# Kernel tuning notes

Measured on AMD Instinct MI355X. Metric: run time of the kernel, lower is better.

## Reference

```python
import jax, jax.numpy as jnp
import numpy as np

B, NQ, NK = 4, 2048, 2048
DQ = DK = DV = 512
H = 8
DS = DV // H  # 64


def _layernorm(x, g, b, eps=1e-5):
    m = jnp.mean(x, axis=-1, keepdims=True)
    v = jnp.var(x, axis=-1, keepdims=True)
    return (x - m) * jax.lax.rsqrt(v + eps) * g + b


def setup_inputs() -> dict:
    key = jax.random.key(0)
    ks = jax.random.split(key, 16)
    def lin(k, fan_in, fan_out):
        # torch nn.Linear default init: U(-1/sqrt(fan_in), 1/sqrt(fan_in))
        bound = 1.0 / np.sqrt(fan_in)
        k1, k2 = jax.random.split(k)
        W = jax.random.uniform(k1, (fan_in, fan_out), jnp.float32, -bound, bound)
        b = jax.random.uniform(k2, (fan_out,), jnp.float32, -bound, bound)
        return W, b
    Wq, bq = lin(ks[0], DQ, DV)
    Wk, bk = lin(ks[1], DK, DV)
    Wv, bv = lin(ks[2], DK, DV)
    W0, b0 = lin(ks[3], DV, DV)
    W1, b1 = lin(ks[4], DV, DV)
    # xavier_uniform for kp/vp of shape (1, DS): bound = sqrt(6/(1+DS))
    xb = np.sqrt(6.0 / (1 + DS))
    kp = jax.random.uniform(ks[5], (DS,), jnp.float32, -xb, xb)
    vp = jax.random.uniform(ks[6], (DS,), jnp.float32, -xb, xb)
    return {
        "Q": jax.random.normal(ks[7], (B, NQ, DQ), jnp.float32),
        "K": jax.random.normal(ks[8], (B, NK, DK), jnp.float32),
        "Kpos": jax.random.uniform(ks[9], (B, NQ, NK), jnp.float32),
        "Wq": Wq, "bq": bq, "Wk": Wk, "bk": bk, "Wv": Wv, "bv": bv,
        "kp": kp, "vp": vp,
        "W0": W0, "b0": b0, "W1": W1, "b1": b1,
        "g0": jnp.ones((DV,), jnp.float32), "be0": jnp.zeros((DV,), jnp.float32),
        "g1": jnp.ones((DV,), jnp.float32), "be1": jnp.zeros((DV,), jnp.float32),
    }


def reference(Q, K, Kpos, Wq, bq, Wk, bk, Wv, bv, kp, vp, W0, b0, W1, b1, g0, be0, g1, be1):
    Qp = Q @ Wq + bq                       # [B,NQ,DV]
    Kp = K @ Wk + bk                       # [B,NK,DV]
    Vp = K @ Wv + bv                       # [B,NK,DV]
    # head split (torch split/cat along batch == reshape to [B,N,H,DS])
    Qh = Qp.reshape(B, NQ, H, DS)
    Kh = Kp.reshape(B, NK, H, DS)
    Vh = Vp.reshape(B, NK, H, DS)
    scale = 1.0 / np.sqrt(DV)              # NOTE: original scales by sqrt(dim_V), not per-head dim
    scores = jnp.einsum('bqhd,bkhd->bhqk', Qh, Kh) * scale
    # ShawRE key bias: KE[b,h,q,k] = Kpos[b,q,k] * <Qh[b,q,h,:], kp>
    qkp = jnp.einsum('bqhd,d->bhq', Qh, kp)          # [B,H,NQ]
    scores = scores + Kpos[:, None, :, :] * qkp[:, :, :, None]
    A = jax.nn.softmax(scores, axis=-1)              # [B,H,NQ,NK]
    out = jnp.einsum('bhqk,bkhd->bqhd', A, Vh)       # [B,NQ,H,DS]
    # ShawRE value bias: VE[b,q,h,:] = (sum_k A*Kpos) * vp
    akp = jnp.einsum('bhqk,bqk->bhq', A, Kpos)       # [B,H,NQ]
    out = out + akp.transpose(0, 2, 1)[..., None] * vp
    O = (Qh + out).reshape(B, NQ, DV)
    O = _layernorm(O, g0, be0)
    resO = O
    O = jax.nn.relu(O @ W0 + b0)           # fc_o[0] with relu (numlayers=2)
    O = resO + jax.nn.relu(O @ W1 + b1)    # fc_o[-1] + residual
    O = _layernorm(O, g1, be1)
    return O
```

## Files before the change

### kernel.cpp

```cpp
#include <hip/hip_runtime.h>
#include <math.h>

#define Bx  4
#define NQx 2048
#define NKx 2048
#define Dx  512
#define Hx  8

typedef __attribute__((ext_vector_type(8))) __bf16 bf16x8;
typedef __attribute__((ext_vector_type(4))) float f32x4;
typedef __attribute__((ext_vector_type(16))) float f32x16;

typedef const __attribute__((address_space(1))) unsigned int* gas_ptr;
typedef __attribute__((address_space(3))) unsigned int* lds_ptr;

__device__ __forceinline__ void gload16(const void* g, void* l){
  __builtin_amdgcn_global_load_lds((gas_ptr)g, (lds_ptr)l, 16, 0, 0);
}

__device__ __forceinline__ unsigned short f2bf(float f){
  union { float f; unsigned int u; } v; v.f = f;
  unsigned int r = (v.u + 0x7FFFu + ((v.u >> 16) & 1u)) >> 16;
  return (unsigned short)r;
}
__device__ __forceinline__ float bf2f(unsigned short u){
  union { unsigned int u; float f; } v; v.u = ((unsigned int)u) << 16; return v.f;
}
__device__ __forceinline__ unsigned int cvtpk_bf16(float a, float b){
  unsigned int d;
  asm("v_cvt_pk_bf16_f32 %0, %1, %2" : "=v"(d) : "v"(a), "v"(b));
  return d;
}
__device__ __forceinline__ void plane32_swap(unsigned int& a, unsigned int& b){
  asm("v_permlane32_swap_b32 %0, %1" : "+v"(a), "+v"(b));
}
__device__ __forceinline__ float fexp2(float x){
  float d; asm("v_exp_f32 %0, %1" : "=v"(d) : "v"(x)); return d;
}
__device__ __forceinline__ float fmax3(float a, float b, float c){
  float d; asm("v_max3_f32 %0, %1, %2, %3" : "=v"(d) : "v"(a), "v"(b), "v"(c)); return d;
}

__global__ __launch_bounds__(256) void mab_wt(
    const float* __restrict__ Wq, const float* __restrict__ Wk, const float* __restrict__ Wv,
    const float* __restrict__ W0, const float* __restrict__ W1,
    unsigned short* __restrict__ Wt)
{
  __shared__ unsigned short T[64][72];
  const int z = blockIdx.z;
  const float* W = (z==0)?Wq:(z==1)?Wk:(z==2)?Wv:(z==3)?W0:W1;
  unsigned short* O = Wt + (size_t)z*512*512;
  const int k0 = blockIdx.x*64, n0 = blockIdx.y*64;
  const int tid = threadIdx.x;
  #pragma unroll
  for (int i=0;i<4;++i){
    int id = tid + i*256;
    int r = id>>4, c4 = id&15;
    float4 v = *(const float4*)(W + (size_t)(k0+r)*512 + n0 + c4*4);
    ushort4 o; o.x=f2bf(v.x); o.y=f2bf(v.y); o.z=f2bf(v.z); o.w=f2bf(v.w);
    *(ushort4*)&T[r][c4*4] = o;
  }
  __syncthreads();
  #pragma unroll
  for (int i=0;i<2;++i){
    int id = tid + i*256;
    int c = id>>3, r8 = id&7;
    union { unsigned short u[8]; uint4 v; } o;
    #pragma unroll
    for (int j=0;j<8;++j) o.u[j] = T[r8*8+j][c];
    *(uint4*)(O + (size_t)(n0+c)*512 + k0 + r8*8) = o.v;
  }
}

__global__ __launch_bounds__(256) void mab_vt(
    const unsigned short* __restrict__ Vp, unsigned short* __restrict__ Vpt)
{
  __shared__ unsigned short T[64][72];
  const int r0 = blockIdx.x*64;
  const int c0 = blockIdx.y*64;
  const int b  = blockIdx.z;
  const int tid = threadIdx.x;
  #pragma unroll
  for (int i=0;i<2;++i){
    int id = tid + i*256;
    int r = id>>3, c8 = id&7;
    *(uint4*)&T[r][c8*8] = *(const uint4*)(Vp + (size_t)(b*NKx + r0+r)*512 + c0 + c8*8);
  }
  __syncthreads();
  #pragma unroll
  for (int i=0;i<2;++i){
    int id = tid + i*256;
    int c = id>>3, r8 = id&7;
    union { unsigned short u[8]; uint4 v; } o;
    #pragma unroll
    for (int j=0;j<8;++j) o.u[j] = T[r8*8+j][c];
    *(uint4*)(Vpt + ((size_t)(b*512) + c0 + c)*NKx + r0 + r8*8) = o.v;
  }
}

__global__ __launch_bounds__(256) void mab_gemm_proj(
    const float* __restrict__ Qf, const float* __restrict__ Kf,
    const unsigned short* __restrict__ Wt,
    const float* __restrict__ bq, const float* __restrict__ bk, const float* __restrict__ bv,
    unsigned short* __restrict__ Cb, float kscale)
{
  __shared__ unsigned short As[128][64];
  __shared__ unsigned short Bs[128][64];
  const int z = blockIdx.z;
  const float* A = (z==0) ? Qf : Kf;
  const unsigned short* W = Wt + (size_t)z*512*512;
  const float* bias = (z==0)?bq:((z==1)?bk:bv);
  const float sc = (z==1) ? kscale : 1.0f;
  const int m0 = blockIdx.y*128, n0 = blockIdx.x*128;
  const int tid = threadIdx.x, w = tid>>6, lane = tid&63, g = lane>>4, q16 = lane&15;
  const int wr = w>>1, wc = w&1;

  f32x4 acc[4][4];
  #pragma unroll
  for (int m=0;m<4;++m)
    #pragma unroll
    for (int n=0;n<4;++n) acc[m][n] = (f32x4){0.f,0.f,0.f,0.f};

  float4 areg[8];
  #pragma unroll
  for (int i=0;i<8;++i){
    int id = i*256 + tid, row = id>>4, qc = id&15;
    areg[i] = *(const float4*)(A + (size_t)(m0+row)*512 + qc*4);
  }

  for (int k0 = 0; k0 < 512; k0 += 64){
    __syncthreads();
    #pragma unroll
    for (int i=0;i<8;++i){
      int id = i*256 + tid, row = id>>4, qc = id&15;
      unsigned int lo = cvtpk_bf16(areg[i].x, areg[i].y);
      unsigned int hi = cvtpk_bf16(areg[i].z, areg[i].w);
      unsigned int* dst = (unsigned int*)((char*)&As[0][0] + row*128
                          + ((qc>>1) ^ (row&7))*16 + (qc&1)*8);
      dst[0] = lo; dst[1] = hi;
    }
    #pragma unroll
    for (int i=0;i<4;++i){
      int o   = (w*4 + i)*1024 + lane*16;
      int row = o >> 7;
      int c   = (o >> 4) & 7;
      int cs  = c ^ (row & 7);
      gload16(W + (size_t)(n0+row)*512 + k0 + cs*8, (char*)&Bs[0][0] + (w*4+i)*1024);
    }
    __syncthreads();
    if (k0 + 64 < 512){
      #pragma unroll
      for (int i=0;i<8;++i){
        int id = i*256 + tid, row = id>>4, qc = id&15;
        areg[i] = *(const float4*)(A + (size_t)(m0+row)*512 + (k0+64) + qc*4);
      }
    }
    #pragma unroll
    for (int ks=0;ks<2;++ks){
      bf16x8 af[4], bfr[4];
      #pragma unroll
      for (int m=0;m<4;++m){
        int row = wr*64 + m*16 + q16;
        int c   = (ks*4 + g) ^ (row & 7);
        af[m] = *(const bf16x8*)((const char*)&As[0][0] + row*128 + c*16);
      }
      #pragma unroll
      for (int n=0;n<4;++n){
        int row = wc*64 + n*16 + q16;
        int c   = (ks*4 + g) ^ (row & 7);
        bfr[n] = *(const bf16x8*)((const char*)&Bs[0][0] + row*128 + c*16);
      }
      #pragma unroll
      for (int m=0;m<4;++m)
        #pragma unroll
        for (int n=0;n<4;++n)
          acc[m][n] = __builtin_amdgcn_mfma_f32_16x16x32_bf16(af[m], bfr[n], acc[m][n], 0,0,0);
    }
  }

  const size_t ZS = (size_t)8192*512;
  #pragma unroll
  for (int m=0;m<4;++m){
    const int rowl = wr*64 + m*16 + g*4;
    #pragma unroll
    for (int n=0;n<4;++n){
      const int col = n0 + wc*64 + n*16 + q16;
      const float bv2 = bias[col];
      #pragma unroll
      for (int r=0;r<4;++r){
        float v = (acc[m][n][r] + bv2) * sc;
        Cb[(size_t)z*ZS + (size_t)(m0 + rowl + r)*512 + col] = f2bf(v);
      }
    }
  }
}

__global__ __launch_bounds__(256) void mab_gemm_mfma(
    const unsigned short* __restrict__ A, const unsigned short* __restrict__ W,
    const float* __restrict__ bias, const float* __restrict__ res,
    unsigned short* __restrict__ Cb, float* __restrict__ Cf, int relu)
{
  __shared__ unsigned short As[128][64];
  __shared__ unsigned short Bs[128][64];
  const int m0 = blockIdx.y*128, n0 = blockIdx.x*128;
  const int tid = threadIdx.x, w = tid>>6, lane = tid&63, g = lane>>4, q16 = lane&15;
  const int wr = w>>1, wc = w&1;

  f32x4 acc[4][4];
  #pragma unroll
  for (int m=0;m<4;++m)
    #pragma unroll
    for (int n=0;n<4;++n) acc[m][n] = (f32x4){0.f,0.f,0.f,0.f};

  for (int k0 = 0; k0 < 512; k0 += 64){
    __syncthreads();
    #pragma unroll
    for (int i=0;i<4;++i){
      int o   = (w*4 + i)*1024 + lane*16;
      int row = o >> 7;
      int c   = (o >> 4) & 7;
      int cs  = c ^ (row & 7);
      gload16(A + (size_t)(m0+row)*512 + k0 + cs*8, (char*)&As[0][0] + (w*4+i)*1024);
      gload16(W + (size_t)(n0+row)*512 + k0 + cs*8, (char*)&Bs[0][0] + (w*4+i)*1024);
    }
    __syncthreads();
    #pragma unroll
    for (int ks=0;ks<2;++ks){
      bf16x8 af[4], bfr[4];
      #pragma unroll
      for (int m=0;m<4;++m){
        int row = wr*64 + m*16 + q16;
        int c   = (ks*4 + g) ^ (row & 7);
        af[m] = *(const bf16x8*)((const char*)&As[0][0] + row*128 + c*16);
      }
      #pragma unroll
      for (int n=0;n<4;++n){
        int row = wc*64 + n*16 + q16;
        int c   = (ks*4 + g) ^ (row & 7);
        bfr[n] = *(const bf16x8*)((const char*)&Bs[0][0] + row*128 + c*16);
      }
      #pragma unroll
      for (int m=0;m<4;++m)
        #pragma unroll
        for (int n=0;n<4;++n)
          acc[m][n] = __builtin_amdgcn_mfma_f32_16x16x32_bf16(af[m], bfr[n], acc[m][n], 0,0,0);
    }
  }

  #pragma unroll
  for (int m=0;m<4;++m){
    const int rowl = wr*64 + m*16 + g*4;
    #pragma unroll
    for (int n=0;n<4;++n){
      const int col = n0 + wc*64 + n*16 + q16;
      const float bv = bias[col];
      #pragma unroll
      for (int r=0;r<4;++r){
        float v = acc[m][n][r] + bv;
        if (relu) v = fmaxf(v, 0.f);
        size_t off = (size_t)(m0 + rowl + r)*512 + col;
        if (res) v += res[off];
        if (Cb) Cb[off] = f2bf(v);
        if (Cf) Cf[off] = v;
      }
    }
  }
}

__global__ __launch_bounds__(256, 4) void mab_attn3(
    const unsigned short* __restrict__ Qp, const unsigned short* __restrict__ Kp,
    const unsigned short* __restrict__ Vpt,
    const float* __restrict__ Kpos, const float* __restrict__ kp, const float* __restrict__ vp,
    float* __restrict__ X)
{
  __shared__ __align__(16) char pool[32768];

  const int q0 = blockIdx.x*64;
  const int h  = blockIdx.y;
  const int b  = blockIdx.z;
  const int tid = threadIdx.x, w = tid>>6, lane = tid&63;
  const int q32 = lane & 31, hi = lane >> 5;
  const int g = w>>1;
  const int qrow = (w&1)*32 + q32;

  char* Kbase = pool + g*16384;
  char* Vbase = pool + g*16384 + 8192;

  const unsigned short* Qg = Qp + ((size_t)(b*NQx + q0))*Dx + h*64;
  const unsigned short* Kg = Kp + ((size_t)b*NKx)*Dx + h*64;
  const unsigned short* Vg = Vpt + ((size_t)(b*512) + h*64)*NKx;
  const float* KProw = Kpos + (size_t)b*NQx*NKx + (size_t)(q0 + qrow)*NKx;

  const int krow0 = lane>>3, kch = lane&7;
  const int vrow0 = lane>>2, vch = lane&3;
  const int shalf = (w&1)*2;

  #pragma unroll
  for (int i=0;i<2;++i){
    int s = shalf + i;
    int kr = s*8 + krow0;
    int kcs = kch ^ (kr & 7);
    gload16(Kg + (size_t)(g*32 + kr)*Dx + kcs*8, Kbase + s*1024);
    int vr = s*16 + vrow0;
    int vcs = vch ^ ((vr>>1) & 3);
    gload16(Vg + (size_t)vr*NKx + g*32 + vcs*8, Vbase + s*1024);
  }

  const unsigned short* Qrowp = Qg + (size_t)qrow*Dx;
  bf16x8 qf[4];
  #pragma unroll
  for (int ds=0; ds<4; ++ds)
    qf[ds] = *(const bf16x8*)(Qrowp + ds*16 + hi*8);

  float qkp = 0.f;
  #pragma unroll
  for (int ds=0; ds<4; ++ds){
    union { bf16x8 v; unsigned short u[8]; } qa; qa.v = qf[ds];
    #pragma unroll
    for (int j=0;j<8;++j)
      qkp = fmaf(bf2f(qa.u[j]), kp[ds*16 + hi*8 + j], qkp);
  }
  qkp += __shfl_xor(qkp, 32);
  qkp *= 1.4426950408889634f;

  float m_i = -1e30f, l_i = 0.f, a_i = 0.f;
  f32x16 accT[2];
  #pragma unroll
  for (int db=0; db<2; ++db)
    #pragma unroll
    for (int r=0;r<16;++r) accT[db][r] = 0.f;

  __syncthreads();

  for (int t = 0; t < 32; ++t){
    const int cur = t & 1;
    const int k0g = t*64 + g*32;

    f32x4 kq[4];
    #pragma unroll
    for (int a=0;a<4;++a)
      kq[a] = *(const f32x4*)(KProw + k0g + a*8 + hi*4);

    if (t < 31){
      const int k1 = k0g + 64;
      #pragma unroll
      for (int i=0;i<2;++i){
        int s = shalf + i;
        int kr = s*8 + krow0;
        int kcs = kch ^ (kr & 7);
        gload16(Kg + (size_t)(k1 + kr)*Dx + kcs*8, Kbase + (cur^1)*4096 + s*1024);
        int vr = s*16 + vrow0;
        int vcs = vch ^ ((vr>>1) & 3);
        gload16(Vg + (size_t)vr*NKx + k1 + vcs*8, Vbase + (cur^1)*4096 + s*1024);
      }
    }
    __builtin_amdgcn_sched_barrier(0);

    f32x16 sT;
    #pragma unroll
    for (int r=0;r<16;++r) sT[r] = 0.f;
    __builtin_amdgcn_s_setprio(1);
    #pragma unroll
    for (int ds=0; ds<4; ++ds){
      int cc = (ds*2 + hi) ^ (q32 & 7);
      bf16x8 kf = *(const bf16x8*)(Kbase + cur*4096 + q32*128 + cc*16);
      sT = __builtin_amdgcn_mfma_f32_32x32x16_bf16(kf, qf[ds], sT, 0,0,0);
    }
    __builtin_amdgcn_s_setprio(0);

    #pragma unroll
    for (int r=0;r<16;++r)
      sT[r] = fmaf(kq[r>>2][r&3], qkp, sT[r]);

    float p0 = fmax3(sT[0],  sT[1],  sT[2]);
    float p1 = fmax3(sT[3],  sT[4],  sT[5]);
    float p2 = fmax3(sT[6],  sT[7],  sT[8]);
    float p3 = fmax3(sT[9],  sT[10], sT[11]);
    float p4 = fmax3(sT[12], sT[13], sT[14]);
    float rm = fmax3(fmax3(p0, p1, p2), fmax3(p3, p4, sT[15]), m_i);
    rm = fmaxf(rm, __shfl_xor(rm, 32));

    if (!__all(rm <= m_i + 11.544f)){
      float al = fexp2(m_i - rm);
      m_i = rm;
      l_i *= al; a_i *= al;
      #pragma unroll
      for (int db=0; db<2; ++db)
        #pragma unroll
        for (int r=0;r<16;++r) accT[db][r] *= al;
    }

    float ps = 0.f, pk = 0.f;
    #pragma unroll
    for (int r=0;r<16;++r){
      float p = fexp2(sT[r] - m_i);
      sT[r] = p;
      ps += p;
      pk = fmaf(p, kq[r>>2][r&3], pk);
    }
    ps += __shfl_xor(ps, 32);
    pk += __shfl_xor(pk, 32);
    l_i += ps; a_i += pk;

    union PW { unsigned int u[4]; bf16x8 v; } pa[2];
    {
      unsigned int w0 = cvtpk_bf16(sT[0],  sT[1]);
      unsigned int w1 = cvtpk_bf16(sT[2],  sT[3]);
      unsigned int w2 = cvtpk_bf16(sT[4],  sT[5]);
      unsigned int w3 = cvtpk_bf16(sT[6],  sT[7]);
      unsigned int w4 = cvtpk_bf16(sT[8],  sT[9]);
      unsigned int w5 = cvtpk_bf16(sT[10], sT[11]);
      unsigned int w6 = cvtpk_bf16(sT[12], sT[13]);
      unsigned int w7 = cvtpk_bf16(sT[14], sT[15]);
      plane32_swap(w0, w2);
      plane32_swap(w1, w3);
      plane32_swap(w4, w6);
      plane32_swap(w5, w7);
      pa[0].u[0]=w0; pa[0].u[1]=w1; pa[0].u[2]=w2; pa[0].u[3]=w3;
      pa[1].u[0]=w4; pa[1].u[1]=w5; pa[1].u[2]=w6; pa[1].u[3]=w7;
    }

    __builtin_amdgcn_s_setprio(1);
    #pragma unroll
    for (int c2=0; c2<2; ++c2){
      #pragma unroll
      for (int db=0; db<2; ++db){
        int row = db*32 + q32;
        int cc  = (c2*2 + hi) ^ ((row>>1) & 3);
        bf16x8 vf = *(const bf16x8*)(Vbase + cur*4096 + row*64 + cc*16);
        accT[db] = __builtin_amdgcn_mfma_f32_32x32x16_bf16(vf, pa[c2].v, accT[db], 0,0,0);
      }
    }
    __builtin_amdgcn_s_setprio(0);

    __syncthreads();
  }

  __syncthreads();
  float* mp = (float*)pool;
  {
    int slot = w*64 + lane;
    float* ms = mp + slot*20;
    int send = 1 - g;
    #pragma unroll
    for (int r=0;r<16;++r) ms[r] = accT[send][r];
    ms[16] = m_i; ms[17] = l_i; ms[18] = a_i;
  }
  __syncthreads();
  {
    int pslot = (w^2)*64 + lane;
    const float* pp = mp + pslot*20;
    float pm = pp[16], pl = pp[17], pav = pp[18];
    float mM = fmaxf(m_i, pm);
    float alS = fexp2(m_i - mM), alP = fexp2(pm - mM);
    float lM = fmaf(l_i, alS, pl*alP);
    float aM = fmaf(a_i, alS, pav*alP);
    float inv = 1.0f / lM;
    float aw  = aM * inv;
    float* Xrow = X + ((size_t)(b*NQx + q0 + qrow))*Dx + h*64;
    #pragma unroll
    for (int a2=0; a2<4; ++a2){
      int d0 = g*32 + a2*8 + hi*4;
      f32x4 vpv = *(const f32x4*)(vp + d0);
      ushort4 qh = *(const ushort4*)(Qrowp + d0);
      float4 o;
      o.x = fmaf(fmaf(accT[g][a2*4+0], alS, pp[a2*4+0]*alP), inv, bf2f(qh.x) + aw*vpv[0]);
      o.y = fmaf(fmaf(accT[g][a2*4+1], alS, pp[a2*4+1]*alP), inv, bf2f(qh.y) + aw*vpv[1]);
      o.z = fmaf(fmaf(accT[g][a2*4+2], alS, pp[a2*4+2]*alP), inv, bf2f(qh.z) + aw*vpv[2]);
      o.w = fmaf(fmaf(accT[g][a2*4+3], alS, pp[a2*4+3]*alP), inv, bf2f(qh.w) + aw*vpv[3]);
      *(float4*)(Xrow + d0) = o;
    }
  }
}

__global__ __launch_bounds__(256) void mab_ln2(
    const float* __restrict__ Xin, const float* __restrict__ g,
    const float* __restrict__ be, float* __restrict__ Yf, unsigned short* __restrict__ Yb)
{
  const int row = blockIdx.x;
  const int tid = threadIdx.x;
  const float* x = Xin + (size_t)row*Dx;
  float2 v = *(const float2*)(x + tid*2);
  float s  = v.x + v.y;
  float sq = fmaf(v.x,v.x, v.y*v.y);
  #pragma unroll
  for (int m=1; m<64; m<<=1){ s += __shfl_xor(s,m); sq += __shfl_xor(sq,m); }
  __shared__ float red[2][4];
  const int wid = tid>>6, lane = tid&63;
  if (lane==0){ red[0][wid]=s; red[1][wid]=sq; }
  __syncthreads();
  s  = red[0][0]+red[0][1]+red[0][2]+red[0][3];
  sq = red[1][0]+red[1][1]+red[1][2]+red[1][3];
  float mean = s*(1.0f/Dx);
  float var  = sq*(1.0f/Dx) - mean*mean;
  float rstd = rsqrtf(var + 1e-5f);
  float2 gg = *(const float2*)(g  + tid*2);
  float2 bb = *(const float2*)(be + tid*2);
  float2 o;
  o.x = (v.x-mean)*rstd*gg.x + bb.x;
  o.y = (v.y-mean)*rstd*gg.y + bb.y;
  if (Yf) *(float2*)(Yf + (size_t)row*Dx + tid*2) = o;
  if (Yb){
    ushort2 ob; ob.x = f2bf(o.x); ob.y = f2bf(o.y);
    *(ushort2*)(Yb + (size_t)row*Dx + tid*2) = ob;
  }
}

extern "C" void kernel_launch(void* const* d_in, const int* in_sizes, int n_in,
                              void* d_out, int out_size, void* d_ws, size_t ws_size,
                              hipStream_t stream)
{
  const float* Q    = (const float*)d_in[0];
  const float* K    = (const float*)d_in[1];
  const float* Kpos = (const float*)d_in[2];
  const float* Wq   = (const float*)d_in[3];
  const float* bq   = (const float*)d_in[4];
  const float* Wk   = (const float*)d_in[5];
  const float* bk   = (const float*)d_in[6];
  const float* Wv   = (const float*)d_in[7];
  const float* bv   = (const float*)d_in[8];
  const float* kp   = (const float*)d_in[9];
  const float* vp   = (const float*)d_in[10];
  const float* W0   = (const float*)d_in[11];
  const float* b0   = (const float*)d_in[12];
  const float* W1   = (const float*)d_in[13];
  const float* b1   = (const float*)d_in[14];
  const float* g0   = (const float*)d_in[15];
  const float* be0  = (const float*)d_in[16];
  const float* g1   = (const float*)d_in[17];
  const float* be1  = (const float*)d_in[18];
  float* out = (float*)d_out;
  char* wsb  = (char*)d_ws;

  const size_t MB = 1024*1024;
  unsigned short* Qp  = (unsigned short*)(wsb);
  unsigned short* Kp  = (unsigned short*)(wsb + 8*MB);
  unsigned short* Vp  = (unsigned short*)(wsb + 16*MB);
  float*          O0  = (float*)         (wsb + 24*MB);
  unsigned short* Vpt = (unsigned short*)(wsb + 40*MB);
  unsigned short* O0b = (unsigned short*)(wsb + 48*MB);
  unsigned short* Wt  = (unsigned short*)(wsb + 56*MB);
  unsigned short* T1  = Vp;

  const float kscale = 0.044194173824159216f * 1.4426950408889634f;

  mab_wt<<<dim3(8,8,5), 256, 0, stream>>>(Wq, Wk, Wv, W0, W1, Wt);
  mab_gemm_proj<<<dim3(4,64,3), 256, 0, stream>>>(Q, K, Wt, bq, bk, bv, Qp, kscale);
  mab_vt<<<dim3(32,8,4), 256, 0, stream>>>(Vp, Vpt);
  mab_attn3<<<dim3(32,8,4), 256, 0, stream>>>(Qp, Kp, Vpt, Kpos, kp, vp, out);
  mab_ln2<<<8192, 256, 0, stream>>>(out, g0, be0, O0, O0b);
  mab_gemm_mfma<<<dim3(4,64,1), 256, 0, stream>>>(
      O0b, Wt + (size_t)3*512*512, b0, nullptr, T1, nullptr, 1);
  mab_gemm_mfma<<<dim3(4,64,1), 256, 0, stream>>>(
      T1, Wt + (size_t)4*512*512, b1, O0, nullptr, out, 1);
  mab_ln2<<<8192, 256, 0, stream>>>(out, g1, be1, out, nullptr);
}
```

Before: 217.8 us.

## Share Kpos tile across all heads in one block; use bf16 residual

The attention kernel is reorganised so each 512-thread block handles 32 queries for all 8 heads, one wave per head. The Kpos tile is staged once in LDS and read by every head, rather than each head block re-reading Kpos from global memory. This removes the 8x redundant Kpos traffic and the cross-wave split-K merge, at the cost of about 136KB of LDS per block and only 256 blocks. The post-LN fp32 copy is dropped, so the residual add now reads the bf16 LN output, which lowers precision on the residual path.

```diff
diff --git a/kernel.cpp b/kernel.cpp
--- a/kernel.cpp
+++ b/kernel.cpp
@@ -197,7 +197,7 @@
 
 __global__ __launch_bounds__(256) void mab_gemm_mfma(
     const unsigned short* __restrict__ A, const unsigned short* __restrict__ W,
-    const float* __restrict__ bias, const float* __restrict__ res,
+    const float* __restrict__ bias, const unsigned short* __restrict__ resb,
     unsigned short* __restrict__ Cb, float* __restrict__ Cf, int relu)
 {
   __shared__ unsigned short As[128][64];
@@ -259,7 +259,7 @@
         float v = acc[m][n][r] + bv;
         if (relu) v = fmaxf(v, 0.f);
         size_t off = (size_t)(m0 + rowl + r)*512 + col;
-        if (res) v += res[off];
+        if (resb) v += bf2f(resb[off]);
         if (Cb) Cb[off] = f2bf(v);
         if (Cf) Cf[off] = v;
       }
@@ -267,46 +267,45 @@
   }
 }
 
-__global__ __launch_bounds__(256, 4) void mab_attn3(
+__global__ __launch_bounds__(512, 2) void mab_attn7(
     const unsigned short* __restrict__ Qp, const unsigned short* __restrict__ Kp,
     const unsigned short* __restrict__ Vpt,
     const float* __restrict__ Kpos, const float* __restrict__ kp, const float* __restrict__ vp,
     float* __restrict__ X)
 {
-  __shared__ __align__(16) char pool[32768];
-
-  const int q0 = blockIdx.x*64;
-  const int h  = blockIdx.y;
-  const int b  = blockIdx.z;
+  __shared__ __align__(16) char pool[139264];
+
+  const int qt = blockIdx.x;
+  const int b  = blockIdx.y;
+  const int q0 = qt*32;
   const int tid = threadIdx.x, w = tid>>6, lane = tid&63;
   const int q32 = lane & 31, hi = lane >> 5;
-  const int g = w>>1;
-  const int qrow = (w&1)*32 + q32;
-
-  char* Kbase = pool + g*16384;
-  char* Vbase = pool + g*16384 + 8192;
-
-  const unsigned short* Qg = Qp + ((size_t)(b*NQx + q0))*Dx + h*64;
+  const int h = w;
+
+  char* Kbase = pool + w*8192;
+  char* Vbase = pool + 65536 + w*8192;
+  char* KQb   = pool + 131072;
+
   const unsigned short* Kg = Kp + ((size_t)b*NKx)*Dx + h*64;
   const unsigned short* Vg = Vpt + ((size_t)(b*512) + h*64)*NKx;
-  const float* KProw = Kpos + (size_t)b*NQx*NKx + (size_t)(q0 + qrow)*NKx;
-
-  const int krow0 = lane>>3, kch = lane&7;
-  const int vrow0 = lane>>2, vch = lane&3;
-  const int shalf = (w&1)*2;
-
-  #pragma unroll
-  for (int i=0;i<2;++i){
-    int s = shalf + i;
-    int kr = s*8 + krow0;
-    int kcs = kch ^ (kr & 7);
-    gload16(Kg + (size_t)(g*32 + kr)*Dx + kcs*8, Kbase + s*1024);
-    int vr = s*16 + vrow0;
-    int vcs = vch ^ ((vr>>1) & 3);
-    gload16(Vg + (size_t)vr*NKx + g*32 + vcs*8, Vbase + s*1024);
-  }
-
-  const unsigned short* Qrowp = Qg + (size_t)qrow*Dx;
+  const float* KPg = Kpos + (size_t)b*NQx*NKx + (size_t)q0*NKx;
+
+  const int sr8 = lane>>3, sc8 = lane&7;
+  const int sr4 = lane>>2, sc4 = lane&3;
+
+  #pragma unroll
+  for (int i=0;i<4;++i){
+    int kr = i*8 + sr8, kcs = sc8 ^ (kr & 7);
+    gload16(Kg + (size_t)kr*Dx + kcs*8, Kbase + i*1024);
+    int vr = i*16 + sr4, vcs = sc4 ^ ((vr>>1) & 3);
+    gload16(Vg + (size_t)vr*NKx + vcs*8, Vbase + i*1024);
+  }
+  if (w < 4){
+    int pr = w*8 + sr8, pcs = sc8 ^ (pr & 7);
+    gload16(KPg + (size_t)pr*NKx + pcs*4, KQb + w*1024);
+  }
+
+  const unsigned short* Qrowp = Qp + ((size_t)(b*NQx + q0 + q32))*Dx + h*64;
   bf16x8 qf[4];
   #pragma unroll
   for (int ds=0; ds<4; ++ds)
@@ -332,26 +331,22 @@
 
   __syncthreads();
 
-  for (int t = 0; t < 32; ++t){
+  for (int t = 0; t < 64; ++t){
     const int cur = t & 1;
-    const int k0g = t*64 + g*32;
-
-    f32x4 kq[4];
-    #pragma unroll
-    for (int a=0;a<4;++a)
-      kq[a] = *(const f32x4*)(KProw + k0g + a*8 + hi*4);
-
-    if (t < 31){
-      const int k1 = k0g + 64;
-      #pragma unroll
-      for (int i=0;i<2;++i){
-        int s = shalf + i;
-        int kr = s*8 + krow0;
-        int kcs = kch ^ (kr & 7);
-        gload16(Kg + (size_t)(k1 + kr)*Dx + kcs*8, Kbase + (cur^1)*4096 + s*1024);
-        int vr = s*16 + vrow0;
-        int vcs = vch ^ ((vr>>1) & 3);
-        gload16(Vg + (size_t)vr*NKx + k1 + vcs*8, Vbase + (cur^1)*4096 + s*1024);
+    const int k0 = t*32;
+
+    if (t+1 < 64){
+      const int k1 = k0 + 32;
+      #pragma unroll
+      for (int i=0;i<4;++i){
+        int kr = i*8 + sr8, kcs = sc8 ^ (kr & 7);
+        gload16(Kg + (size_t)(k1 + kr)*Dx + kcs*8, Kbase + (cur^1)*4096 + i*1024);
+        int vr = i*16 + sr4, vcs = sc4 ^ ((vr>>1) & 3);
+        gload16(Vg + (size_t)vr*NKx + k1 + vcs*8, Vbase + (cur^1)*4096 + i*1024);
+      }
+      if (w < 4){
+        int pr = w*8 + sr8, pcs = sc8 ^ (pr & 7);
+        gload16(KPg + (size_t)pr*NKx + k1 + pcs*4, KQb + (cur^1)*4096 + w*1024);
       }
     }
     __builtin_amdgcn_sched_barrier(0);
@@ -368,16 +363,23 @@
     }
     __builtin_amdgcn_s_setprio(0);
 
+    f32x4 kq[4];
+    #pragma unroll
+    for (int a=0;a<4;++a){
+      int cc = (a*2 + hi) ^ (q32 & 7);
+      kq[a] = *(const f32x4*)(KQb + cur*4096 + q32*128 + cc*16);
+    }
+
     #pragma unroll
     for (int r=0;r<16;++r)
       sT[r] = fmaf(kq[r>>2][r&3], qkp, sT[r]);
 
-    float p0 = fmax3(sT[0],  sT[1],  sT[2]);
-    float p1 = fmax3(sT[3],  sT[4],  sT[5]);
-    float p2 = fmax3(sT[6],  sT[7],  sT[8]);
-    float p3 = fmax3(sT[9],  sT[10], sT[11]);
-    float p4 = fmax3(sT[12], sT[13], sT[14]);
-    float rm = fmax3(fmax3(p0, p1, p2), fmax3(p3, p4, sT[15]), m_i);
+    float t0 = fmax3(sT[0],  sT[1],  sT[2]);
+    float t1 = fmax3(sT[3],  sT[4],  sT[5]);
+    float t2 = fmax3(sT[6],  sT[7],  sT[8]);
+    float t3 = fmax3(sT[9],  sT[10], sT[11]);
+    float t4 = fmax3(sT[12], sT[13], sT[14]);
+    float rm = fmax3(fmax3(t0, t1, t2), fmax3(t3, t4, sT[15]), m_i);
     rm = fmaxf(rm, __shfl_xor(rm, 32));
 
     if (!__all(rm <= m_i + 11.544f)){
@@ -390,14 +392,17 @@
         for (int r=0;r<16;++r) accT[db][r] *= al;
     }
 
-    float ps = 0.f, pk = 0.f;
+    float psq[4] = {0.f,0.f,0.f,0.f};
+    float pkq[4] = {0.f,0.f,0.f,0.f};
     #pragma unroll
     for (int r=0;r<16;++r){
       float p = fexp2(sT[r] - m_i);
       sT[r] = p;
-      ps += p;
-      pk = fmaf(p, kq[r>>2][r&3], pk);
-    }
+      psq[r&3] += p;
+      pkq[r&3] = fmaf(p, kq[r>>2][r&3], pkq[r&3]);
+    }
+    float ps = (psq[0]+psq[1]) + (psq[2]+psq[3]);
+    float pk = (pkq[0]+pkq[1]) + (pkq[2]+pkq[3]);
     ps += __shfl_xor(ps, 32);
     pk += __shfl_xor(pk, 32);
     l_i += ps; a_i += pk;
@@ -436,38 +441,21 @@
     __syncthreads();
   }
 
-  __syncthreads();
-  float* mp = (float*)pool;
-  {
-    int slot = w*64 + lane;
-    float* ms = mp + slot*20;
-    int send = 1 - g;
-    #pragma unroll
-    for (int r=0;r<16;++r) ms[r] = accT[send][r];
-    ms[16] = m_i; ms[17] = l_i; ms[18] = a_i;
-  }
-  __syncthreads();
-  {
-    int pslot = (w^2)*64 + lane;
-    const float* pp = mp + pslot*20;
-    float pm = pp[16], pl = pp[17], pav = pp[18];
-    float mM = fmaxf(m_i, pm);
-    float alS = fexp2(m_i - mM), alP = fexp2(pm - mM);
-    float lM = fmaf(l_i, alS, pl*alP);
-    float aM = fmaf(a_i, alS, pav*alP);
-    float inv = 1.0f / lM;
-    float aw  = aM * inv;
-    float* Xrow = X + ((size_t)(b*NQx + q0 + qrow))*Dx + h*64;
+  float inv = 1.0f / l_i;
+  float aw  = a_i * inv;
+  float* Xrow = X + ((size_t)(b*NQx + q0 + q32))*Dx + h*64;
+  #pragma unroll
+  for (int db=0; db<2; ++db){
     #pragma unroll
     for (int a2=0; a2<4; ++a2){
-      int d0 = g*32 + a2*8 + hi*4;
+      int d0 = db*32 + a2*8 + hi*4;
       f32x4 vpv = *(const f32x4*)(vp + d0);
       ushort4 qh = *(const ushort4*)(Qrowp + d0);
       float4 o;
-      o.x = fmaf(fmaf(accT[g][a2*4+0], alS, pp[a2*4+0]*alP), inv, bf2f(qh.x) + aw*vpv[0]);
-      o.y = fmaf(fmaf(accT[g][a2*4+1], alS, pp[a2*4+1]*alP), inv, bf2f(qh.y) + aw*vpv[1]);
-      o.z = fmaf(fmaf(accT[g][a2*4+2], alS, pp[a2*4+2]*alP), inv, bf2f(qh.z) + aw*vpv[2]);
-      o.w = fmaf(fmaf(accT[g][a2*4+3], alS, pp[a2*4+3]*alP), inv, bf2f(qh.w) + aw*vpv[3]);
+      o.x = fmaf(accT[db][a2*4+0], inv, bf2f(qh.x) + aw*vpv[0]);
+      o.y = fmaf(accT[db][a2*4+1], inv, bf2f(qh.y) + aw*vpv[1]);
+      o.z = fmaf(accT[db][a2*4+2], inv, bf2f(qh.z) + aw*vpv[2]);
+      o.w = fmaf(accT[db][a2*4+3], inv, bf2f(qh.w) + aw*vpv[3]);
       *(float4*)(Xrow + d0) = o;
     }
   }
@@ -536,10 +524,9 @@
   unsigned short* Qp  = (unsigned short*)(wsb);
   unsigned short* Kp  = (unsigned short*)(wsb + 8*MB);
   unsigned short* Vp  = (unsigned short*)(wsb + 16*MB);
-  float*          O0  = (float*)         (wsb + 24*MB);
-  unsigned short* Vpt = (unsigned short*)(wsb + 40*MB);
-  unsigned short* O0b = (unsigned short*)(wsb + 48*MB);
-  unsigned short* Wt  = (unsigned short*)(wsb + 56*MB);
+  unsigned short* Vpt = (unsigned short*)(wsb + 24*MB);
+  unsigned short* O0b = (unsigned short*)(wsb + 32*MB);
+  unsigned short* Wt  = (unsigned short*)(wsb + 40*MB);
   unsigned short* T1  = Vp;
 
   const float kscale = 0.044194173824159216f * 1.4426950408889634f;
@@ -547,11 +534,11 @@
   mab_wt<<<dim3(8,8,5), 256, 0, stream>>>(Wq, Wk, Wv, W0, W1, Wt);
   mab_gemm_proj<<<dim3(4,64,3), 256, 0, stream>>>(Q, K, Wt, bq, bk, bv, Qp, kscale);
   mab_vt<<<dim3(32,8,4), 256, 0, stream>>>(Vp, Vpt);
-  mab_attn3<<<dim3(32,8,4), 256, 0, stream>>>(Qp, Kp, Vpt, Kpos, kp, vp, out);
-  mab_ln2<<<8192, 256, 0, stream>>>(out, g0, be0, O0, O0b);
+  mab_attn7<<<dim3(64,4), 512, 0, stream>>>(Qp, Kp, Vpt, Kpos, kp, vp, out);
+  mab_ln2<<<8192, 256, 0, stream>>>(out, g0, be0, nullptr, O0b);
   mab_gemm_mfma<<<dim3(4,64,1), 256, 0, stream>>>(
       O0b, Wt + (size_t)3*512*512, b0, nullptr, T1, nullptr, 1);
   mab_gemm_mfma<<<dim3(4,64,1), 256, 0, stream>>>(
-      T1, Wt + (size_t)4*512*512, b1, O0, nullptr, out, 1);
+      T1, Wt + (size_t)4*512*512, b1, O0b, nullptr, out, 1);
   mab_ln2<<<8192, 256, 0, stream>>>(out, g1, be1, out, nullptr);
 }
```

Result: faster. 207.2 us (-4.9%).
